# Optimization experiments

Measured on AMD Instinct MI355X. Metric: run time of the kernel, lower is better.

The kernel has to match this reference:

```python
import jax, jax.numpy as jnp
import numpy as np

BOX = 8.0  # side length of the box points are sampled in
N_POINTS = 12288
N_BINS_TARGET = 10


def setup_inputs() -> dict:
    key = jax.random.key(0)
    k1, k2 = jax.random.split(key)
    pc = jax.random.uniform(k1, (N_POINTS, 3), dtype=jnp.float32) * BOX
    target_rdf = jax.random.uniform(k2, (N_BINS_TARGET,), dtype=jnp.float32) * 2.0
    return {"reconstructed_pc": pc, "target_rdf": target_rdf, "r_max": 10, "dr": 1.0}


def _calculate_rdf(pc, r_max, dr):
    # pc: [N, 3]. r_max, dr are static Python scalars.
    n = pc.shape[0]
    nbins = int(round(float(r_max) / float(dr)))  # len(arange(0, r_max+dr, dr)) - 1
    # Pairwise Euclidean distances via the Gram-matrix trick (same math as torch.cdist p=2).
    sq = jnp.sum(pc * pc, axis=1)                               # [N]
    d2 = sq[:, None] + sq[None, :] - 2.0 * (pc @ pc.T)          # [N, N]
    d = jnp.sqrt(jnp.maximum(d2, 0.0)).ravel()                  # [N*N]
    # torch.histc(bins=nbins, min=0, max=r_max): uniform bins, max value inclusive in last bin.
    idx = jnp.clip(jnp.floor(d / dr).astype(jnp.int32), 0, nbins - 1)
    w = (d <= r_max).astype(jnp.float32)                        # d >= 0 always holds
    hist = jax.ops.segment_sum(w, idx, num_segments=nbins)      # [nbins]
    r_mid = (jnp.arange(nbins, dtype=jnp.float32) + 0.5) * dr
    density = n / (4.0 / 3.0 * jnp.pi * float(r_max) ** 3)
    ideal_counts = 4.0 * jnp.pi * r_mid ** 2 * dr * density * n
    rdf = hist / ideal_counts
    rdf = jnp.where(jnp.isnan(rdf), 0.0, rdf)
    return rdf, r_mid


def reference(reconstructed_pc, target_rdf, r_max, dr):
    rdf, _ = _calculate_rdf(reconstructed_pc, r_max, dr)
    m = min(int(target_rdf.shape[0]), int(rdf.shape[0]))
    diff = rdf[:m] - target_rdf[:m]
    return jnp.mean(diff * diff)
```

## Files before the change

kernel.cpp:

```cpp
#include <hip/hip_runtime.h>


#define BLOCK    256
#define IBLK     4
#define ITILE    (BLOCK * IBLK)
#define JCH      64
#define NB       10
#define SLOT     16
#define FP32_SAT 16777216u

template <bool STRADDLE>
__device__ __forceinline__ void jloop(const float4* __restrict__ sj,
                                      const float* sqi, const float* m2x,
                                      const float* m2y, const float* m2z,
                                      const int* iidx, int jbase,
                                      unsigned int* c)
{
    for (int jc = 0; jc < JCH; jc += 8) {
        unsigned long long cnt = 0ull;
        #pragma unroll
        for (int jj = 0; jj < 8; ++jj) {
            const int j = jc + jj;
            float4 p = sj[j];
            #pragma unroll
            for (int r = 0; r < IBLK; ++r) {
                float d2 = sqi[r] + p.w;
                d2 = fmaf(m2x[r], p.x, d2);
                d2 = fmaf(m2y[r], p.y, d2);
                d2 = fmaf(m2z[r], p.z, d2);
                if (STRADDLE) d2 = (jbase + j > iidx[r]) ? d2 : 3.0e30f;
                float d = __builtin_amdgcn_sqrtf(d2);
                unsigned int b = (unsigned int)d;
                b = min(b, 10u);
                cnt += 1ull << (b * 6u);
            }
        }
        #pragma unroll
        for (int k = 0; k < NB; ++k)
            c[k] += (unsigned int)(cnt >> (6 * k)) & 63u;
    }
}

__global__ __launch_bounds__(BLOCK) void rdf_hist_kernel(
    const float* __restrict__ pc, const int* __restrict__ rmaxp,
    const float* __restrict__ drp, unsigned int* __restrict__ part, int n)
{
    const int I  = (int)blockIdx.x;
    const int Jc = (int)blockIdx.y;
    const int jbase = Jc * JCH;
    const int ibase = I * ITILE;
    if (jbase + JCH - 1 <= ibase) return;

    __shared__ float4 sj[JCH];
    __shared__ unsigned int sacc[NB];

    const int tid = threadIdx.x;
    const float inv_dr = 1.0f / (*drp);

    if (tid < NB) sacc[tid] = 0u;
    if (tid < JCH) {
        const int j = jbase + tid;
        float x = -3.0e4f, y = -3.0e4f, z = -3.0e4f;
        if (j < n) { x = pc[3*j] * inv_dr; y = pc[3*j+1] * inv_dr; z = pc[3*j+2] * inv_dr; }
        sj[tid] = make_float4(x, y, z, x*x + y*y + z*z);
    }

    float sqi[IBLK], m2x[IBLK], m2y[IBLK], m2z[IBLK];
    int iidx[IBLK];
    #pragma unroll
    for (int r = 0; r < IBLK; ++r) {
        const int i = ibase + tid + BLOCK * r;
        iidx[r] = i;
        float x = 3.0e4f, y = 3.0e4f, z = 3.0e4f;
        if (i < n) { x = pc[3*i] * inv_dr; y = pc[3*i+1] * inv_dr; z = pc[3*i+2] * inv_dr; }
        sqi[r] = x*x + y*y + z*z;
        m2x[r] = -2.f * x; m2y[r] = -2.f * y; m2z[r] = -2.f * z;
    }

    __syncthreads();

    unsigned int c[NB];
    #pragma unroll
    for (int k = 0; k < NB; ++k) c[k] = 0u;

    if (jbase <= ibase + ITILE - 1)
        jloop<true >(sj, sqi, m2x, m2y, m2z, iidx, jbase, c);
    else
        jloop<false>(sj, sqi, m2x, m2y, m2z, iidx, jbase, c);

    #pragma unroll
    for (int k = 0; k < NB; ++k) {
        unsigned int s = c[k];
        #pragma unroll
        for (int m = 32; m >= 1; m >>= 1) s += (unsigned int)__shfl_xor((int)s, m, 64);
        c[k] = s;
    }
    if ((tid & 63) == 0) {
        #pragma unroll
        for (int k = 0; k < NB; ++k) atomicAdd(&sacc[k], c[k]);
    }
    __syncthreads();
    const int bid = (int)blockIdx.x + (int)gridDim.x * (int)blockIdx.y;
    if (tid < NB) part[bid * SLOT + tid] = sacc[tid];
}

__global__ __launch_bounds__(BLOCK) void rdf_reduce_loss_kernel(
    const unsigned int* __restrict__ part, const float* __restrict__ target,
    const int* __restrict__ rmaxp, const float* __restrict__ drp,
    float* __restrict__ out, int n, int mt, int nI, int nJ)
{
    __shared__ unsigned int sacc[NB];
    const int tid = threadIdx.x;
    if (tid < NB) sacc[tid] = 0u;
    __syncthreads();

    unsigned int a[NB];
    #pragma unroll
    for (int k = 0; k < NB; ++k) a[k] = 0u;
    const int nslots = nI * nJ;
    for (int s = tid; s < nslots; s += BLOCK) {
        const int I  = s % nI;
        const int Jc = s / nI;
        if (Jc * JCH + JCH - 1 > I * ITILE) {
            #pragma unroll
            for (int k = 0; k < NB; ++k) a[k] += part[s * SLOT + k];
        }
    }
    #pragma unroll
    for (int k = 0; k < NB; ++k) {
        unsigned int s = a[k];
        #pragma unroll
        for (int m = 32; m >= 1; m >>= 1) s += (unsigned int)__shfl_xor((int)s, m, 64);
        if ((tid & 63) == 0) atomicAdd(&sacc[k], s);
    }
    __syncthreads();

    if (tid == 0) {
        const float PI = 3.14159265358979323846f;
        const float rmax = (float)(*rmaxp);
        const float dr   = *drp;
        int nbins = (int)roundf(rmax / dr);
        if (nbins > NB) nbins = NB;
        const float density = (float)n / (4.0f / 3.0f * PI * rmax * rmax * rmax);
        const int m = (mt < nbins) ? mt : nbins;
        float acc = 0.0f;
        for (int b = 0; b < m; ++b) {
            unsigned int hb = 2u * sacc[b] + ((b == 0) ? (unsigned int)n : 0u);
            if (hb > FP32_SAT) hb = FP32_SAT;
            float r_mid = ((float)b + 0.5f) * dr;
            float ideal = 4.0f * PI * r_mid * r_mid * dr * density * (float)n;
            float rdf  = (ideal != 0.0f) ? ((float)hb / ideal) : 0.0f;
            float diff = rdf - target[b];
            acc = fmaf(diff, diff, acc);
        }
        out[0] = acc / (float)m;
    }
}

extern "C" void kernel_launch(void* const* d_in, const int* in_sizes, int n_in,
                              void* d_out, int out_size, void* d_ws, size_t ws_size,
                              hipStream_t stream)
{
    const float* pc     = (const float*)d_in[0];
    const float* target = (const float*)d_in[1];
    const int*   rmaxp  = (const int*)d_in[2];
    const float* drp    = (const float*)d_in[3];
    const int n  = in_sizes[0] / 3;
    const int mt = in_sizes[1];

    unsigned int* part = (unsigned int*)d_ws;
    const int nI = (n + ITILE - 1) / ITILE;
    const int nJ = (n + JCH - 1) / JCH;

    dim3 grid(nI, nJ);
    rdf_hist_kernel<<<grid, BLOCK, 0, stream>>>(pc, rmaxp, drp, part, n);
    rdf_reduce_loss_kernel<<<1, BLOCK, 0, stream>>>(part, target, rmaxp, drp,
                                                    (float*)d_out, n, mt, nI, nJ);
}
```

Baseline: 47.50 us.

## Launch only upper-triangle tiles via 1D grid with quadratic index mapping

Replaces the 2D grid, where roughly half the blocks exited early below the diagonal, with a compact 1D grid that enumerates only the needed (i-tile, j-chunk) pairs. Each block recovers its tile from the block index by solving a quadratic and then correcting with a short loop. The global loads of point coordinates are also issued before the shared-memory setup, so that their latency can overlap. The reduce kernel now sums a dense partial array and no longer needs the per-slot triangle test. The cost is some extra integer and float math per block to decode its tile.

```diff
diff --git a/kernel.cpp b/kernel.cpp
--- a/kernel.cpp
+++ b/kernel.cpp
@@ -5,9 +5,14 @@
 #define IBLK     4
 #define ITILE    (BLOCK * IBLK)
 #define JCH      64
+#define DJC      (ITILE / JCH)
 #define NB       10
 #define SLOT     16
 #define FP32_SAT 16777216u
+
+__device__ __forceinline__ int pre_rows(int k, int njc) {
+    return k * njc - (DJC / 2) * k * (k - 1);
+}
 
 template <bool STRADDLE>
 __device__ __forceinline__ void jloop(const float4* __restrict__ sj,
@@ -16,11 +21,11 @@
                                       const int* iidx, int jbase,
                                       unsigned int* c)
 {
-    for (int jc = 0; jc < JCH; jc += 8) {
+    for (int jc0 = 0; jc0 < JCH; jc0 += 8) {
         unsigned long long cnt = 0ull;
         #pragma unroll
         for (int jj = 0; jj < 8; ++jj) {
-            const int j = jc + jj;
+            const int j = jc0 + jj;
             float4 p = sj[j];
             #pragma unroll
             for (int r = 0; r < IBLK; ++r) {
@@ -43,36 +48,53 @@
 
 __global__ __launch_bounds__(BLOCK) void rdf_hist_kernel(
     const float* __restrict__ pc, const int* __restrict__ rmaxp,
-    const float* __restrict__ drp, unsigned int* __restrict__ part, int n)
+    const float* __restrict__ drp, unsigned int* __restrict__ part,
+    int n, int nI, int njc)
 {
-    const int I  = (int)blockIdx.x;
-    const int Jc = (int)blockIdx.y;
-    const int jbase = Jc * JCH;
-    const int ibase = I * ITILE;
-    if (jbase + JCH - 1 <= ibase) return;
-
     __shared__ float4 sj[JCH];
     __shared__ unsigned int sacc[NB];
 
     const int tid = threadIdx.x;
+    const int bid = (int)blockIdx.x;
+
+    const float a  = (float)(DJC / 2);
+    const float bq = (float)njc + a;
+    float disc = bq * bq - 4.0f * a * (float)bid;
+    disc = fmaxf(disc, 0.0f);
+    int k = (int)((bq - sqrtf(disc)) / (2.0f * a));
+    k = max(0, min(k, nI - 1));
+    while (k > 0 && pre_rows(k, njc) > bid) --k;
+    while (k + 1 < nI && pre_rows(k + 1, njc) <= bid) ++k;
+    const int jc    = (bid - pre_rows(k, njc)) + DJC * k;
+    const int ibase = k * ITILE;
+    const int jbase = jc * JCH;
+
     const float inv_dr = 1.0f / (*drp);
 
-    if (tid < NB) sacc[tid] = 0u;
+    float jx = -3.0e4f, jy = -3.0e4f, jz = -3.0e4f;
     if (tid < JCH) {
         const int j = jbase + tid;
-        float x = -3.0e4f, y = -3.0e4f, z = -3.0e4f;
-        if (j < n) { x = pc[3*j] * inv_dr; y = pc[3*j+1] * inv_dr; z = pc[3*j+2] * inv_dr; }
-        sj[tid] = make_float4(x, y, z, x*x + y*y + z*z);
+        if (j < n) { jx = pc[3*j]; jy = pc[3*j+1]; jz = pc[3*j+2]; }
     }
-
-    float sqi[IBLK], m2x[IBLK], m2y[IBLK], m2z[IBLK];
+    float rx[IBLK], ry[IBLK], rz[IBLK];
     int iidx[IBLK];
     #pragma unroll
     for (int r = 0; r < IBLK; ++r) {
         const int i = ibase + tid + BLOCK * r;
         iidx[r] = i;
-        float x = 3.0e4f, y = 3.0e4f, z = 3.0e4f;
-        if (i < n) { x = pc[3*i] * inv_dr; y = pc[3*i+1] * inv_dr; z = pc[3*i+2] * inv_dr; }
+        rx[r] = 3.0e4f; ry[r] = 3.0e4f; rz[r] = 3.0e4f;
+        if (i < n) { rx[r] = pc[3*i]; ry[r] = pc[3*i+1]; rz[r] = pc[3*i+2]; }
+    }
+
+    if (tid < NB) sacc[tid] = 0u;
+    if (tid < JCH) {
+        const float x = jx * inv_dr, y = jy * inv_dr, z = jz * inv_dr;
+        sj[tid] = make_float4(x, y, z, x*x + y*y + z*z);
+    }
+    float sqi[IBLK], m2x[IBLK], m2y[IBLK], m2z[IBLK];
+    #pragma unroll
+    for (int r = 0; r < IBLK; ++r) {
+        const float x = rx[r] * inv_dr, y = ry[r] * inv_dr, z = rz[r] * inv_dr;
         sqi[r] = x*x + y*y + z*z;
         m2x[r] = -2.f * x; m2y[r] = -2.f * y; m2z[r] = -2.f * z;
     }
@@ -81,33 +103,32 @@
 
     unsigned int c[NB];
     #pragma unroll
-    for (int k = 0; k < NB; ++k) c[k] = 0u;
+    for (int q = 0; q < NB; ++q) c[q] = 0u;
 
-    if (jbase <= ibase + ITILE - 1)
+    if (jbase < ibase + ITILE)
         jloop<true >(sj, sqi, m2x, m2y, m2z, iidx, jbase, c);
     else
         jloop<false>(sj, sqi, m2x, m2y, m2z, iidx, jbase, c);
 
     #pragma unroll
-    for (int k = 0; k < NB; ++k) {
-        unsigned int s = c[k];
+    for (int q = 0; q < NB; ++q) {
+        unsigned int s = c[q];
         #pragma unroll
         for (int m = 32; m >= 1; m >>= 1) s += (unsigned int)__shfl_xor((int)s, m, 64);
-        c[k] = s;
+        c[q] = s;
     }
     if ((tid & 63) == 0) {
         #pragma unroll
-        for (int k = 0; k < NB; ++k) atomicAdd(&sacc[k], c[k]);
+        for (int q = 0; q < NB; ++q) atomicAdd(&sacc[q], c[q]);
     }
     __syncthreads();
-    const int bid = (int)blockIdx.x + (int)gridDim.x * (int)blockIdx.y;
     if (tid < NB) part[bid * SLOT + tid] = sacc[tid];
 }
 
 __global__ __launch_bounds__(BLOCK) void rdf_reduce_loss_kernel(
     const unsigned int* __restrict__ part, const float* __restrict__ target,
     const int* __restrict__ rmaxp, const float* __restrict__ drp,
-    float* __restrict__ out, int n, int mt, int nI, int nJ)
+    float* __restrict__ out, int n, int mt, int nblocks)
 {
     __shared__ unsigned int sacc[NB];
     const int tid = threadIdx.x;
@@ -116,22 +137,17 @@
 
     unsigned int a[NB];
     #pragma unroll
-    for (int k = 0; k < NB; ++k) a[k] = 0u;
-    const int nslots = nI * nJ;
-    for (int s = tid; s < nslots; s += BLOCK) {
-        const int I  = s % nI;
-        const int Jc = s / nI;
-        if (Jc * JCH + JCH - 1 > I * ITILE) {
-            #pragma unroll
-            for (int k = 0; k < NB; ++k) a[k] += part[s * SLOT + k];
-        }
+    for (int q = 0; q < NB; ++q) a[q] = 0u;
+    for (int s = tid; s < nblocks; s += BLOCK) {
+        #pragma unroll
+        for (int q = 0; q < NB; ++q) a[q] += part[s * SLOT + q];
     }
     #pragma unroll
-    for (int k = 0; k < NB; ++k) {
-        unsigned int s = a[k];
+    for (int q = 0; q < NB; ++q) {
+        unsigned int s = a[q];
         #pragma unroll
         for (int m = 32; m >= 1; m >>= 1) s += (unsigned int)__shfl_xor((int)s, m, 64);
-        if ((tid & 63) == 0) atomicAdd(&sacc[k], s);
+        if ((tid & 63) == 0) atomicAdd(&sacc[q], s);
     }
     __syncthreads();
 
@@ -169,11 +185,11 @@
     const int mt = in_sizes[1];
 
     unsigned int* part = (unsigned int*)d_ws;
-    const int nI = (n + ITILE - 1) / ITILE;
-    const int nJ = (n + JCH - 1) / JCH;
+    const int nI  = (n + ITILE - 1) / ITILE;
+    const int njc = (n + JCH - 1) / JCH;
+    const int nblocks = nI * njc - (DJC / 2) * nI * (nI - 1);
 
-    dim3 grid(nI, nJ);
-    rdf_hist_kernel<<<grid, BLOCK, 0, stream>>>(pc, rmaxp, drp, part, n);
+    rdf_hist_kernel<<<nblocks, BLOCK, 0, stream>>>(pc, rmaxp, drp, part, n, nI, njc);
     rdf_reduce_loss_kernel<<<1, BLOCK, 0, stream>>>(part, target, rmaxp, drp,
-                                                    (float*)d_out, n, mt, nI, nJ);
+                                                    (float*)d_out, n, mt, nblocks);
 }
```

Result: faster. 41.61 us (-12.4%).
